# Kernel optimization log

Hardware: AMD Instinct MI355X
Metric: run time of the kernel (lower is better)

The kernel has to match this reference:

```python
import jax, jax.numpy as jnp
import numpy as np

HEADS = 16
D_MODEL = 1024
D_HEAD = D_MODEL // HEADS


def setup_inputs() -> dict:
    key = jax.random.key(0)
    ks = jax.random.split(key, 9)
    s_h = 1.0 / np.sqrt(D_HEAD)
    s_m = 1.0 / np.sqrt(D_MODEL)
    return {
        "x": jax.random.normal(ks[0], (4, 2048, D_MODEL), dtype=jnp.float32),
        "Wq": jax.random.uniform(ks[1], (D_HEAD, D_HEAD), jnp.float32, -s_h, s_h),
        "bq": jax.random.uniform(ks[2], (D_HEAD,), jnp.float32, -s_h, s_h),
        "Wk": jax.random.uniform(ks[3], (D_HEAD, D_HEAD), jnp.float32, -s_h, s_h),
        "bk": jax.random.uniform(ks[4], (D_HEAD,), jnp.float32, -s_h, s_h),
        "Wv": jax.random.uniform(ks[5], (D_HEAD, D_HEAD), jnp.float32, -s_h, s_h),
        "bv": jax.random.uniform(ks[6], (D_HEAD,), jnp.float32, -s_h, s_h),
        "Wp": jax.random.uniform(ks[7], (D_MODEL, D_MODEL), jnp.float32, -s_m, s_m),
        "bp": jax.random.uniform(ks[8], (D_MODEL,), jnp.float32, -s_m, s_m),
    }


def reference(x, Wq, bq, Wk, bk, Wv, bv, Wp, bp):
    B, T, C = x.shape
    xh = x.reshape(B, T, HEADS, D_HEAD)  # [B,T,H,Dh]
    # per-head linear projections (torch Linear: x @ W.T + b)
    q = jnp.einsum('bthd,ed->bhte', xh, Wq) + bq  # [B,H,T,Dh]
    k = jnp.einsum('bthd,ed->bhte', xh, Wk) + bk
    v = jnp.einsum('bthd,ed->bhte', xh, Wv) + bv
    # NOTE: original scales by sqrt(C) = sqrt(d_model), not sqrt(d_head)
    att = jnp.einsum('bhqd,bhkd->bhqk', q, k) / jnp.sqrt(jnp.float32(C))
    att = jax.nn.softmax(att, axis=-1)
    out = jnp.einsum('bhqk,bhkd->bhqd', att, v)  # [B,H,T,Dh]
    out = out.transpose(0, 2, 1, 3).reshape(B, T, C)
    return out @ Wp.T + bp
```

## Files before the change

### kernel.cpp

```cpp
#include <hip/hip_runtime.h>
#include <hip/hip_bf16.h>
#include <cstddef>

#define B_  4
#define T_  2048
#define H_  16
#define DH  64
#define C_  1024
#define BH  64

typedef float  f32x16 __attribute__((ext_vector_type(16)));
typedef __bf16 bf16x8 __attribute__((ext_vector_type(8)));

#define MFMA32(a, b, c) __builtin_amdgcn_mfma_f32_32x32x16_bf16(a, b, c, 0, 0, 0)


__global__ __launch_bounds__(256) void qkv_kernel(
    const float* __restrict__ x,
    const float* __restrict__ Wq, const float* __restrict__ bq,
    const float* __restrict__ Wk, const float* __restrict__ bk,
    const float* __restrict__ Wv, const float* __restrict__ bv,
    __bf16* __restrict__ q, __bf16* __restrict__ k, __bf16* __restrict__ vt)
{
    __shared__ __bf16 Xs[128 * 72];
    __shared__ __bf16 Ws[3][64 * 72];
    __bf16* Vtl = Xs;

    const int tt  = blockIdx.x;
    const int bh  = blockIdx.y;
    const int b   = bh >> 4, h = bh & 15;
    const int t0  = tt * 128;
    const int tid = threadIdx.x;
    const int wave = tid >> 6, lane = tid & 63;
    const int m = lane & 31, hh = lane >> 5;

    #pragma unroll
    for (int i = 0; i < 8; ++i) {
        const int idx = i * 256 + tid;
        const int r = idx >> 4, c = (idx & 15) * 4;
        const float4 x4 = *(const float4*)(x + ((size_t)(b * T_ + t0 + r)) * C_ + h * DH + c);
        const uint lo = ((uint)__builtin_bit_cast(unsigned short, (__bf16)x4.y) << 16)
                      | (uint)__builtin_bit_cast(unsigned short, (__bf16)x4.x);
        const uint hi = ((uint)__builtin_bit_cast(unsigned short, (__bf16)x4.w) << 16)
                      | (uint)__builtin_bit_cast(unsigned short, (__bf16)x4.z);
        *(uint*)&Xs[r * 72 + c]     = lo;
        *(uint*)&Xs[r * 72 + c + 2] = hi;
    }
    #pragma unroll
    for (int i = 0; i < 4; ++i) {
        const int idx = i * 256 + tid;
        const int r = idx >> 4, c = (idx & 15) * 4;
        const float* wsrc[3] = {Wq, Wk, Wv};
        #pragma unroll
        for (int wv_ = 0; wv_ < 3; ++wv_) {
            const float4 w4 = *(const float4*)(wsrc[wv_] + r * 64 + c);
            const uint lo = ((uint)__builtin_bit_cast(unsigned short, (__bf16)w4.y) << 16)
                          | (uint)__builtin_bit_cast(unsigned short, (__bf16)w4.x);
            const uint hi = ((uint)__builtin_bit_cast(unsigned short, (__bf16)w4.w) << 16)
                          | (uint)__builtin_bit_cast(unsigned short, (__bf16)w4.z);
            *(uint*)&Ws[wv_][r * 72 + c]     = lo;
            *(uint*)&Ws[wv_][r * 72 + c + 2] = hi;
        }
    }
    __syncthreads();

    bf16x8 xf[4];
    #pragma unroll
    for (int ks = 0; ks < 4; ++ks)
        xf[ks] = *(const bf16x8*)&Xs[(wave * 32 + m) * 72 + ks * 16 + hh * 8];
    __syncthreads();

    const float s32 = 0.03125f;

    #pragma unroll
    for (int mat = 0; mat < 3; ++mat) {
        f32x16 acc0 = {}, acc1 = {};
        #pragma unroll
        for (int ks = 0; ks < 4; ++ks) {
            const bf16x8 w0 = *(const bf16x8*)&Ws[mat][(m) * 72 + ks * 16 + hh * 8];
            const bf16x8 w1 = *(const bf16x8*)&Ws[mat][(32 + m) * 72 + ks * 16 + hh * 8];
            acc0 = MFMA32(xf[ks], w0, acc0);
            acc1 = MFMA32(xf[ks], w1, acc1);
        }
        const float* bias = (mat == 0) ? bq : (mat == 1) ? bk : bv;
        const float b0 = bias[m], b1 = bias[32 + m];
        #pragma unroll
        for (int r = 0; r < 16; ++r) {
            const int R = (r & 3) + 8 * (r >> 2) + 4 * hh;
            const int tloc = wave * 32 + R;
            const float v0 = acc0[r] + b0, v1 = acc1[r] + b1;
            if (mat == 0) {
                const size_t base = ((size_t)bh * T_ + t0 + tloc) * DH;
                q[base + m]      = (__bf16)(v0 * s32);
                q[base + 32 + m] = (__bf16)(v1 * s32);
            } else if (mat == 1) {
                const size_t base = ((size_t)bh * T_ + t0 + tloc) * DH;
                k[base + m]      = (__bf16)v0;
                k[base + 32 + m] = (__bf16)v1;
            } else {
                Vtl[(m) * 136 + tloc]      = (__bf16)v0;
                Vtl[(32 + m) * 136 + tloc] = (__bf16)v1;
            }
        }
    }
    __syncthreads();
    #pragma unroll
    for (int i = 0; i < 4; ++i) {
        const int idx = i * 256 + tid;
        const int e = idx >> 4, c = (idx & 15) * 8;
        *(uint4*)(vt + ((size_t)(bh * 64 + e)) * T_ + t0 + c) = *(uint4*)&Vtl[e * 136 + c];
    }
}

__global__ __launch_bounds__(256, 3) void attn_kernel(
    const __bf16* __restrict__ q, const __bf16* __restrict__ k,
    const __bf16* __restrict__ vt, __bf16* __restrict__ o)
{
    __shared__ __bf16 Ks[64 * 72];
    __shared__ __bf16 Vts[64 * 72];
    __shared__ __bf16 Ps[128 * 72];

    const int bh  = blockIdx.y;
    const int q0  = blockIdx.x * 128;
    const int tid = threadIdx.x;
    const int wave = tid >> 6, lane = tid & 63;
    const int m = lane & 31, h = lane >> 5;
    const int qrow0 = wave * 32;

    const __bf16* qb = q  + (size_t)bh * T_ * DH;
    const __bf16* kb = k  + (size_t)bh * T_ * DH;
    const __bf16* vb = vt + (size_t)bh * DH * T_;

    #pragma unroll
    for (int i = 0; i < 4; ++i) {
        const int idx = i * 256 + tid;
        const int r = idx >> 3, c = (idx & 7) * 8;
        *(uint4*)&Ps[r * 72 + c] = *(const uint4*)(qb + (size_t)(q0 + r) * DH + c);
    }
    __syncthreads();

    bf16x8 qf[4];
    #pragma unroll
    for (int ks = 0; ks < 4; ++ks)
        qf[ks] = *(const bf16x8*)&Ps[(qrow0 + m) * 72 + ks * 16 + h * 8];

    f32x16 O0 = {}, O1 = {};
    float lsum[16];
    #pragma unroll
    for (int r = 0; r < 16; ++r) lsum[r] = 0.f;

    for (int kt = 0; kt < T_; kt += 64) {
        __syncthreads();
        #pragma unroll
        for (int i = 0; i < 2; ++i) {
            const int idx = i * 256 + tid;
            const int r = idx >> 3, c = (idx & 7) * 8;
            *(uint4*)&Ks[r * 72 + c] = *(const uint4*)(kb + (size_t)(kt + r) * DH + c);
        }
        #pragma unroll
        for (int i = 0; i < 2; ++i) {
            const int idx = i * 256 + tid;
            const int r = idx >> 3, c = (idx & 7) * 8;
            *(uint4*)&Vts[r * 72 + c] = *(const uint4*)(vb + (size_t)r * T_ + kt + c);
        }
        __syncthreads();

        f32x16 S0 = {}, S1 = {};
        #pragma unroll
        for (int ks = 0; ks < 4; ++ks) {
            const bf16x8 k0 = *(const bf16x8*)&Ks[(m) * 72 + ks * 16 + h * 8];
            const bf16x8 k1 = *(const bf16x8*)&Ks[(32 + m) * 72 + ks * 16 + h * 8];
            S0 = MFMA32(qf[ks], k0, S0);
            S1 = MFMA32(qf[ks], k1, S1);
        }

        #pragma unroll
        for (int r = 0; r < 16; ++r) {
            const int R = (r & 3) + 8 * (r >> 2) + 4 * h;
            const float p0 = __expf(S0[r]);
            const float p1 = __expf(S1[r]);
            lsum[r] += p0 + p1;
            Ps[(qrow0 + R) * 72 + m]      = (__bf16)p0;
            Ps[(qrow0 + R) * 72 + 32 + m] = (__bf16)p1;
        }

        #pragma unroll
        for (int ks = 0; ks < 4; ++ks) {
            const bf16x8 pf = *(const bf16x8*)&Ps[(qrow0 + m) * 72 + ks * 16 + h * 8];
            const bf16x8 v0 = *(const bf16x8*)&Vts[(m) * 72 + ks * 16 + h * 8];
            const bf16x8 v1 = *(const bf16x8*)&Vts[(32 + m) * 72 + ks * 16 + h * 8];
            O0 = MFMA32(pf, v0, O0);
            O1 = MFMA32(pf, v1, O1);
        }
    }

    #pragma unroll
    for (int r = 0; r < 16; ++r) {
        float s = lsum[r];
        s += __shfl_xor(s, 1);  s += __shfl_xor(s, 2);  s += __shfl_xor(s, 4);
        s += __shfl_xor(s, 8);  s += __shfl_xor(s, 16);
        lsum[r] = 1.0f / s;
    }
    __bf16* ob = o + (size_t)bh * T_ * DH;
    #pragma unroll
    for (int r = 0; r < 16; ++r) {
        const int R = (r & 3) + 8 * (r >> 2) + 4 * h;
        const size_t row = (size_t)(q0 + qrow0 + R) * DH;
        ob[row + m]      = (__bf16)(O0[r] * lsum[r]);
        ob[row + 32 + m] = (__bf16)(O1[r] * lsum[r]);
    }
}

__global__ __launch_bounds__(256) void proj_kernel(
    const __bf16* __restrict__ a,
    const float* __restrict__ Wp, const float* __restrict__ bp,
    float* __restrict__ out)
{
    __shared__ __bf16 As[128 * 72];
    __shared__ __bf16 Bs[128 * 72];

    const int tb = blockIdx.x, eb = blockIdx.y;
    const int tid = threadIdx.x;
    const int wave = tid >> 6, lane = tid & 63;
    const int m = lane & 31, h = lane >> 5;
    const int tok0 = tb * 128;
    const int b = tok0 >> 11, t0 = tok0 & (T_ - 1);
    const int e0 = eb * 128;

    f32x16 acc[4] = {f32x16{}, f32x16{}, f32x16{}, f32x16{}};

    for (int cb = 0; cb < 16; ++cb) {
        __syncthreads();
        #pragma unroll
        for (int i = 0; i < 4; ++i) {
            const int idx = i * 256 + tid;
            const int r = idx >> 3, c = (idx & 7) * 8;
            *(uint4*)&As[r * 72 + c] =
                *(const uint4*)(a + ((size_t)(b * H_ + cb) * T_ + t0 + r) * DH + c);
        }
        #pragma unroll
        for (int i = 0; i < 8; ++i) {
            const int idx = i * 256 + tid;
            const int r = idx >> 4, c = (idx & 15) * 4;
            const float4 w4 = *(const float4*)(Wp + (size_t)(e0 + r) * C_ + cb * 64 + c);
            const uint lo = ((uint)__builtin_bit_cast(unsigned short, (__bf16)w4.y) << 16)
                          | (uint)__builtin_bit_cast(unsigned short, (__bf16)w4.x);
            const uint hi = ((uint)__builtin_bit_cast(unsigned short, (__bf16)w4.w) << 16)
                          | (uint)__builtin_bit_cast(unsigned short, (__bf16)w4.z);
            *(uint*)&Bs[r * 72 + c]     = lo;
            *(uint*)&Bs[r * 72 + c + 2] = hi;
        }
        __syncthreads();

        #pragma unroll
        for (int ks = 0; ks < 4; ++ks) {
            const bf16x8 af = *(const bf16x8*)&As[(wave * 32 + m) * 72 + ks * 16 + h * 8];
            #pragma unroll
            for (int n = 0; n < 4; ++n) {
                const bf16x8 bf = *(const bf16x8*)&Bs[(n * 32 + m) * 72 + ks * 16 + h * 8];
                acc[n] = MFMA32(af, bf, acc[n]);
            }
        }
    }

    #pragma unroll
    for (int n = 0; n < 4; ++n) {
        const int e = e0 + n * 32 + m;
        const float bias = bp[e];
        #pragma unroll
        for (int r = 0; r < 16; ++r) {
            const int R = (r & 3) + 8 * (r >> 2) + 4 * h;
            out[(size_t)(tok0 + wave * 32 + R) * C_ + e] = acc[n][r] + bias;
        }
    }
}

extern "C" void kernel_launch(void* const* d_in, const int* in_sizes, int n_in,
                              void* d_out, int out_size, void* d_ws, size_t ws_size,
                              hipStream_t stream)
{
    const float* x  = (const float*)d_in[0];
    const float* Wq = (const float*)d_in[1];
    const float* bq = (const float*)d_in[2];
    const float* Wk = (const float*)d_in[3];
    const float* bk = (const float*)d_in[4];
    const float* Wv = (const float*)d_in[5];
    const float* bv = (const float*)d_in[6];
    const float* Wp = (const float*)d_in[7];
    const float* bp = (const float*)d_in[8];

    const size_t N = (size_t)BH * T_ * DH;
    __bf16* qws  = (__bf16*)d_ws;
    __bf16* kws  = qws + N;
    __bf16* vtws = kws + N;
    __bf16* ows  = vtws + N;

    qkv_kernel<<<dim3(16, 64), 256, 0, stream>>>(
        x, Wq, bq, Wk, bk, Wv, bv, qws, kws, vtws);
    attn_kernel<<<dim3(16, 64), 256, 0, stream>>>(qws, kws, vtws, ows);
    proj_kernel<<<dim3(64, 8), 256, 0, stream>>>(ows, Wp, bp, (float*)d_out);
}
```

Before: 234.9 us.

## Preconvert Wp to bf16 in qkv kernel, use exp2 with folded log2e scale

The qkv kernel also converts the projection weight Wp to bf16 into workspace, so the projection kernel loads bf16 tiles directly instead of converting fp32 on every tile. The Q scale now folds in log2(e) so attention can use exp2f instead of __expf. In the attention kernel, K rows are interleaved (2m, 2m+1) so each lane's two probabilities pack into one 32-bit LDS store, and the K and V tile loads are merged into one loop. These cut redundant conversion work and LDS store count, but require extra workspace and depend on the K row permutation matching the packed P layout.

```diff
diff --git a/kernel.cpp b/kernel.cpp
--- a/kernel.cpp
+++ b/kernel.cpp
@@ -15,11 +15,17 @@
 #define MFMA32(a, b, c) __builtin_amdgcn_mfma_f32_32x32x16_bf16(a, b, c, 0, 0, 0)
 
 
+__device__ __forceinline__ unsigned pack2(float a, float b) {
+    return ((unsigned)__builtin_bit_cast(unsigned short, (__bf16)b) << 16)
+         | (unsigned)__builtin_bit_cast(unsigned short, (__bf16)a);
+}
+
 __global__ __launch_bounds__(256) void qkv_kernel(
     const float* __restrict__ x,
     const float* __restrict__ Wq, const float* __restrict__ bq,
     const float* __restrict__ Wk, const float* __restrict__ bk,
     const float* __restrict__ Wv, const float* __restrict__ bv,
+    const float* __restrict__ Wp, __bf16* __restrict__ Wp16,
     __bf16* __restrict__ q, __bf16* __restrict__ k, __bf16* __restrict__ vt)
 {
     __shared__ __bf16 Xs[128 * 72];
@@ -34,17 +40,20 @@
     const int wave = tid >> 6, lane = tid & 63;
     const int m = lane & 31, hh = lane >> 5;
 
+    {
+        const int flat = (bh * 16 + tt) * 256 + tid;
+        const float4 w4 = *(const float4*)(Wp + (size_t)flat * 4);
+        uint2 pk; pk.x = pack2(w4.x, w4.y); pk.y = pack2(w4.z, w4.w);
+        *(uint2*)(Wp16 + (size_t)flat * 4) = pk;
+    }
+
     #pragma unroll
     for (int i = 0; i < 8; ++i) {
         const int idx = i * 256 + tid;
         const int r = idx >> 4, c = (idx & 15) * 4;
         const float4 x4 = *(const float4*)(x + ((size_t)(b * T_ + t0 + r)) * C_ + h * DH + c);
-        const uint lo = ((uint)__builtin_bit_cast(unsigned short, (__bf16)x4.y) << 16)
-                      | (uint)__builtin_bit_cast(unsigned short, (__bf16)x4.x);
-        const uint hi = ((uint)__builtin_bit_cast(unsigned short, (__bf16)x4.w) << 16)
-                      | (uint)__builtin_bit_cast(unsigned short, (__bf16)x4.z);
-        *(uint*)&Xs[r * 72 + c]     = lo;
-        *(uint*)&Xs[r * 72 + c + 2] = hi;
+        *(unsigned*)&Xs[r * 72 + c]     = pack2(x4.x, x4.y);
+        *(unsigned*)&Xs[r * 72 + c + 2] = pack2(x4.z, x4.w);
     }
     #pragma unroll
     for (int i = 0; i < 4; ++i) {
@@ -54,12 +63,8 @@
         #pragma unroll
         for (int wv_ = 0; wv_ < 3; ++wv_) {
             const float4 w4 = *(const float4*)(wsrc[wv_] + r * 64 + c);
-            const uint lo = ((uint)__builtin_bit_cast(unsigned short, (__bf16)w4.y) << 16)
-                          | (uint)__builtin_bit_cast(unsigned short, (__bf16)w4.x);
-            const uint hi = ((uint)__builtin_bit_cast(unsigned short, (__bf16)w4.w) << 16)
-                          | (uint)__builtin_bit_cast(unsigned short, (__bf16)w4.z);
-            *(uint*)&Ws[wv_][r * 72 + c]     = lo;
-            *(uint*)&Ws[wv_][r * 72 + c + 2] = hi;
+            *(unsigned*)&Ws[wv_][r * 72 + c]     = pack2(w4.x, w4.y);
+            *(unsigned*)&Ws[wv_][r * 72 + c + 2] = pack2(w4.z, w4.w);
         }
     }
     __syncthreads();
@@ -70,7 +75,7 @@
         xf[ks] = *(const bf16x8*)&Xs[(wave * 32 + m) * 72 + ks * 16 + hh * 8];
     __syncthreads();
 
-    const float s32 = 0.03125f;
+    const float sQ = 0.03125f * 1.44269504f;
 
     #pragma unroll
     for (int mat = 0; mat < 3; ++mat) {
@@ -91,8 +96,8 @@
             const float v0 = acc0[r] + b0, v1 = acc1[r] + b1;
             if (mat == 0) {
                 const size_t base = ((size_t)bh * T_ + t0 + tloc) * DH;
-                q[base + m]      = (__bf16)(v0 * s32);
-                q[base + 32 + m] = (__bf16)(v1 * s32);
+                q[base + m]      = (__bf16)(v0 * sQ);
+                q[base + 32 + m] = (__bf16)(v1 * sQ);
             } else if (mat == 1) {
                 const size_t base = ((size_t)bh * T_ + t0 + tloc) * DH;
                 k[base + m]      = (__bf16)v0;
@@ -116,9 +121,9 @@
     const __bf16* __restrict__ q, const __bf16* __restrict__ k,
     const __bf16* __restrict__ vt, __bf16* __restrict__ o)
 {
+    __shared__ __bf16 PQs[128 * 72];
     __shared__ __bf16 Ks[64 * 72];
     __shared__ __bf16 Vts[64 * 72];
-    __shared__ __bf16 Ps[128 * 72];
 
     const int bh  = blockIdx.y;
     const int q0  = blockIdx.x * 128;
@@ -135,14 +140,14 @@
     for (int i = 0; i < 4; ++i) {
         const int idx = i * 256 + tid;
         const int r = idx >> 3, c = (idx & 7) * 8;
-        *(uint4*)&Ps[r * 72 + c] = *(const uint4*)(qb + (size_t)(q0 + r) * DH + c);
+        *(uint4*)&PQs[r * 72 + c] = *(const uint4*)(qb + (size_t)(q0 + r) * DH + c);
     }
     __syncthreads();
 
     bf16x8 qf[4];
     #pragma unroll
     for (int ks = 0; ks < 4; ++ks)
-        qf[ks] = *(const bf16x8*)&Ps[(qrow0 + m) * 72 + ks * 16 + h * 8];
+        qf[ks] = *(const bf16x8*)&PQs[(qrow0 + m) * 72 + ks * 16 + h * 8];
 
     f32x16 O0 = {}, O1 = {};
     float lsum[16];
@@ -155,12 +160,7 @@
         for (int i = 0; i < 2; ++i) {
             const int idx = i * 256 + tid;
             const int r = idx >> 3, c = (idx & 7) * 8;
-            *(uint4*)&Ks[r * 72 + c] = *(const uint4*)(kb + (size_t)(kt + r) * DH + c);
-        }
-        #pragma unroll
-        for (int i = 0; i < 2; ++i) {
-            const int idx = i * 256 + tid;
-            const int r = idx >> 3, c = (idx & 7) * 8;
+            *(uint4*)&Ks[r * 72 + c]  = *(const uint4*)(kb + (size_t)(kt + r) * DH + c);
             *(uint4*)&Vts[r * 72 + c] = *(const uint4*)(vb + (size_t)r * T_ + kt + c);
         }
         __syncthreads();
@@ -168,8 +168,8 @@
         f32x16 S0 = {}, S1 = {};
         #pragma unroll
         for (int ks = 0; ks < 4; ++ks) {
-            const bf16x8 k0 = *(const bf16x8*)&Ks[(m) * 72 + ks * 16 + h * 8];
-            const bf16x8 k1 = *(const bf16x8*)&Ks[(32 + m) * 72 + ks * 16 + h * 8];
+            const bf16x8 k0 = *(const bf16x8*)&Ks[(2 * m) * 72 + ks * 16 + h * 8];
+            const bf16x8 k1 = *(const bf16x8*)&Ks[(2 * m + 1) * 72 + ks * 16 + h * 8];
             S0 = MFMA32(qf[ks], k0, S0);
             S1 = MFMA32(qf[ks], k1, S1);
         }
@@ -177,16 +177,15 @@
         #pragma unroll
         for (int r = 0; r < 16; ++r) {
             const int R = (r & 3) + 8 * (r >> 2) + 4 * h;
-            const float p0 = __expf(S0[r]);
-            const float p1 = __expf(S1[r]);
+            const float p0 = exp2f(S0[r]);
+            const float p1 = exp2f(S1[r]);
             lsum[r] += p0 + p1;
-            Ps[(qrow0 + R) * 72 + m]      = (__bf16)p0;
-            Ps[(qrow0 + R) * 72 + 32 + m] = (__bf16)p1;
-        }
-
-        #pragma unroll
-        for (int ks = 0; ks < 4; ++ks) {
-            const bf16x8 pf = *(const bf16x8*)&Ps[(qrow0 + m) * 72 + ks * 16 + h * 8];
+            *(unsigned*)&PQs[(qrow0 + R) * 72 + 2 * m] = pack2(p0, p1);
+        }
+
+        #pragma unroll
+        for (int ks = 0; ks < 4; ++ks) {
+            const bf16x8 pf = *(const bf16x8*)&PQs[(qrow0 + m) * 72 + ks * 16 + h * 8];
             const bf16x8 v0 = *(const bf16x8*)&Vts[(m) * 72 + ks * 16 + h * 8];
             const bf16x8 v1 = *(const bf16x8*)&Vts[(32 + m) * 72 + ks * 16 + h * 8];
             O0 = MFMA32(pf, v0, O0);
@@ -213,7 +212,7 @@
 
 __global__ __launch_bounds__(256) void proj_kernel(
     const __bf16* __restrict__ a,
-    const float* __restrict__ Wp, const float* __restrict__ bp,
+    const __bf16* __restrict__ Wp16, const float* __restrict__ bp,
     float* __restrict__ out)
 {
     __shared__ __bf16 As[128 * 72];
@@ -237,18 +236,8 @@
             const int r = idx >> 3, c = (idx & 7) * 8;
             *(uint4*)&As[r * 72 + c] =
                 *(const uint4*)(a + ((size_t)(b * H_ + cb) * T_ + t0 + r) * DH + c);
-        }
-        #pragma unroll
-        for (int i = 0; i < 8; ++i) {
-            const int idx = i * 256 + tid;
-            const int r = idx >> 4, c = (idx & 15) * 4;
-            const float4 w4 = *(const float4*)(Wp + (size_t)(e0 + r) * C_ + cb * 64 + c);
-            const uint lo = ((uint)__builtin_bit_cast(unsigned short, (__bf16)w4.y) << 16)
-                          | (uint)__builtin_bit_cast(unsigned short, (__bf16)w4.x);
-            const uint hi = ((uint)__builtin_bit_cast(unsigned short, (__bf16)w4.w) << 16)
-                          | (uint)__builtin_bit_cast(unsigned short, (__bf16)w4.z);
-            *(uint*)&Bs[r * 72 + c]     = lo;
-            *(uint*)&Bs[r * 72 + c + 2] = hi;
+            *(uint4*)&Bs[r * 72 + c] =
+                *(const uint4*)(Wp16 + (size_t)(e0 + r) * C_ + cb * 64 + c);
         }
         __syncthreads();
 
@@ -294,9 +283,10 @@
     __bf16* kws  = qws + N;
     __bf16* vtws = kws + N;
     __bf16* ows  = vtws + N;
+    __bf16* wp16 = ows + N;
 
     qkv_kernel<<<dim3(16, 64), 256, 0, stream>>>(
-        x, Wq, bq, Wk, bk, Wv, bv, qws, kws, vtws);
+        x, Wq, bq, Wk, bk, Wv, bv, Wp, wp16, qws, kws, vtws);
     attn_kernel<<<dim3(16, 64), 256, 0, stream>>>(qws, kws, vtws, ows);
-    proj_kernel<<<dim3(64, 8), 256, 0, stream>>>(ows, Wp, bp, (float*)d_out);
-}
+    proj_kernel<<<dim3(64, 8), 256, 0, stream>>>(ows, wp16, bp, (float*)d_out);
+}
```

Measured after the change: 264.8 us. 12.7% more time.
